# Kernel tuning notes

Measured on AMD Instinct MI355X. Metric: run time of the kernel, lower is better.

The kernel has to match this reference:

```python
import jax, jax.numpy as jnp
import numpy as np

N_NODES = 100000
N_EDGES = 1000000
NFEAT = 64
NHID = 64
NCLASS = 10
DROPOUT = 0.3
PAE_HID = 128  # hidden width of PAE in HOGCN/EV-GCN
EPS_BN = 1e-5
EPS_COS = 1e-8


def setup_inputs() -> dict:
    key = jax.random.key(0)
    ks = jax.random.split(key, 16)
    def w(k, shape, fan_in):
        return jax.random.normal(k, shape, dtype=jnp.float32) * (1.0 / np.sqrt(fan_in))
    inp = {
        "x": jax.random.normal(ks[0], (N_NODES, NFEAT), dtype=jnp.float32),
        "edge_index": jax.random.randint(ks[1], (2, N_EDGES), 0, N_NODES, dtype=jnp.int32),
        "edgenet_input": jax.random.normal(ks[2], (N_EDGES, 4), dtype=jnp.float32),
        # PAE params: Linear(2,128) -> ReLU -> BN(128) -> Dropout -> Linear(128,128)
        "pae_w1": w(ks[3], (2, PAE_HID), 2),
        "pae_b1": jnp.zeros((PAE_HID,), jnp.float32),
        "pae_gamma": jnp.ones((PAE_HID,), jnp.float32),
        "pae_beta": jnp.zeros((PAE_HID,), jnp.float32),
        "pae_w2": w(ks[4], (PAE_HID, PAE_HID), PAE_HID),
        "pae_b2": jnp.zeros((PAE_HID,), jnp.float32),
        # GCNConv layers
        "conv1_w": w(ks[5], (NFEAT, NHID), NFEAT),
        "conv1_b": jnp.zeros((NHID,), jnp.float32),
        "conv2_w": w(ks[6], (NHID, NHID), NHID),
        "conv2_b": jnp.zeros((NHID,), jnp.float32),
        # MLP head
        "lin1_w": w(ks[7], (NHID, NHID // 2), NHID),
        "lin1_b": jnp.zeros((NHID // 2,), jnp.float32),
        "lin2_w": w(ks[8], (NHID // 2, NCLASS), NHID // 2),
        "lin2_b": jnp.zeros((NCLASS,), jnp.float32),
    }
    return inp


def _pae(edgenet_input, w1, b1, gamma, beta, w2, b2, key):
    # Split edge input into the two endpoint halves; run shared parser on both.
    d = edgenet_input.shape[1] // 2
    x12 = jnp.stack([edgenet_input[:, :d], edgenet_input[:, d:]], axis=0)  # [2, E, d]
    h = jax.nn.relu(x12 @ w1 + b1)  # [2, E, H]
    # BatchNorm1d (training mode): stats over the edge batch, per parser call
    mean = h.mean(axis=1, keepdims=True)
    var = h.var(axis=1, keepdims=True)
    h = (h - mean) * jax.lax.rsqrt(var + EPS_BN) * gamma + beta
    keep = jax.random.bernoulli(key, 1.0 - DROPOUT, h.shape)
    h = jnp.where(keep, h / (1.0 - DROPOUT), 0.0)
    h = h @ w2 + b2
    h1, h2 = h[0], h[1]
    n1 = jnp.maximum(jnp.linalg.norm(h1, axis=-1), EPS_COS)
    n2 = jnp.maximum(jnp.linalg.norm(h2, axis=-1), EPS_COS)
    cos = (h1 * h2).sum(-1) / (n1 * n2)
    return (cos + 1.0) * 0.5  # [E]


def _gcn_conv(x, row, col, ew, W, b, n):
    # PyG GCNConv: add self-loops (weight 1), symmetric normalization, then
    # gather-scale-scatter aggregation of linearly transformed features.
    xw = x @ W  # [N, out]
    sl = jnp.arange(n, dtype=row.dtype)
    row_f = jnp.concatenate([row, sl])
    col_f = jnp.concatenate([col, sl])
    ew_f = jnp.concatenate([ew, jnp.ones((n,), ew.dtype)])
    deg = jax.ops.segment_sum(ew_f, col_f, num_segments=n)
    dinv = jnp.where(deg > 0, jax.lax.rsqrt(jnp.maximum(deg, 1e-12)), 0.0)
    norm = dinv[row_f] * ew_f * dinv[col_f]  # [E+N]
    msgs = norm[:, None] * xw[row_f]  # irregular gather + scale
    out = jax.ops.segment_sum(msgs, col_f, num_segments=n)  # scatter-add
    return out + b


def reference(x, edge_index, edgenet_input,
              pae_w1, pae_b1, pae_gamma, pae_beta, pae_w2, pae_b2,
              conv1_w, conv1_b, conv2_w, conv2_b,
              lin1_w, lin1_b, lin2_w, lin2_b):
    n = x.shape[0]
    row, col = edge_index[0], edge_index[1]
    k_pae, k_head = jax.random.split(jax.random.key(42))
    edge_weight = _pae(edgenet_input, pae_w1, pae_b1, pae_gamma, pae_beta,
                       pae_w2, pae_b2, k_pae)
    h = jax.nn.relu(_gcn_conv(x, row, col, edge_weight, conv1_w, conv1_b, n))
    h = jax.nn.relu(_gcn_conv(h, row, col, edge_weight, conv2_w, conv2_b, n))
    h = jax.nn.relu(h @ lin1_w + lin1_b)
    keep = jax.random.bernoulli(k_head, 1.0 - DROPOUT, h.shape)
    h = jnp.where(keep, h / (1.0 - DROPOUT), 0.0)
    out = h @ lin2_w + lin2_b
    return out
```

## Files before the change

### kernel.cpp

```cpp
#include <hip/hip_runtime.h>
#include <stdint.h>


#define NN 100000
#define NE 1000000
#define INV_KEEP (1.0f/0.7f)
#define KEEP_THR 3006477312u

#define BN_BLOCKS   1000
#define HIST_BLOCKS 3907
#define PAE_BLOCKS  31250
#define XW1_BLOCKS  1563
#define MEGA_GROUPS 782
#define MEGA_BLOCKS (MEGA_GROUPS * 47)

typedef short bf16x8 __attribute__((ext_vector_type(8)));
typedef float f32x4  __attribute__((ext_vector_type(4)));
typedef uint32_t u32x4 __attribute__((ext_vector_type(4)));

__host__ __device__ constexpr uint32_t rotl32c(uint32_t x, int r) {
  return (x << r) | (x >> (32 - r));
}

struct TFK { uint32_t a, b; };
__host__ __device__ constexpr TFK tf_const(uint32_t k0, uint32_t k1,
                                           uint32_t x0, uint32_t x1) {
  uint32_t k2 = k0 ^ k1 ^ 0x1BD11BDAu;
  x0 += k0; x1 += k1;
#define TFC_R(r) { x0 += x1; x1 = rotl32c(x1, (r)); x1 ^= x0; }
  TFC_R(13) TFC_R(15) TFC_R(26) TFC_R(6)   x0 += k1; x1 += k2 + 1u;
  TFC_R(17) TFC_R(29) TFC_R(16) TFC_R(24)  x0 += k2; x1 += k0 + 2u;
  TFC_R(13) TFC_R(15) TFC_R(26) TFC_R(6)   x0 += k0; x1 += k1 + 3u;
  TFC_R(17) TFC_R(29) TFC_R(16) TFC_R(24)  x0 += k1; x1 += k2 + 4u;
  TFC_R(13) TFC_R(15) TFC_R(26) TFC_R(6)   x0 += k2; x1 += k0 + 5u;
#undef TFC_R
  return TFK{x0, x1};
}

constexpr TFK KP = tf_const(0u, 42u, 0u, 0u);
constexpr TFK KH = tf_const(0u, 42u, 0u, 1u);

template <uint32_t K0, uint32_t K1>
__device__ __forceinline__ uint32_t tf_bits(uint32_t idx) {
  constexpr uint32_t K2 = K0 ^ K1 ^ 0x1BD11BDAu;
  uint32_t x0 = K0;
  uint32_t x1 = idx + K1;
#define TF_R(r) { x0 += x1; \
    x1 = __builtin_amdgcn_alignbit(x1, x1, 32u - (r)) ^ x0; }
  TF_R(13) TF_R(15) TF_R(26) TF_R(6)   x0 += K1; x1 += K2 + 1u;
  TF_R(17) TF_R(29) TF_R(16) TF_R(24)  x0 += K2; x1 += K0 + 2u;
  TF_R(13) TF_R(15) TF_R(26) TF_R(6)   x0 += K0; x1 += K1 + 3u;
  TF_R(17) TF_R(29) TF_R(16) TF_R(24)  x0 += K1; x1 += K2 + 4u;
  TF_R(13) TF_R(15) TF_R(26) TF_R(6)   x0 += K2; x1 += K0 + 5u;
#undef TF_R
  return x0 ^ x1;
}

__device__ __forceinline__ uint16_t f2bf(float f) {
  uint32_t u = __float_as_uint(f);
  return (uint16_t)((u + 0x7FFFu + ((u >> 16) & 1u)) >> 16);
}

__device__ __forceinline__ float bf2f(uint16_t u) {
  return __uint_as_float((uint32_t)u << 16);
}

__global__ __launch_bounds__(256) void phase1(const float* __restrict__ edgenet,
                                              const float* __restrict__ w1,
                                              const float* __restrict__ b1,
                                              const int* __restrict__ colp,
                                              float* __restrict__ sums,
                                              int* __restrict__ cnt) {
  int b = blockIdx.x;
  int t = threadIdx.x;
  if (b < BN_BLOCKS) {
    int c = t & 127, g = t >> 7;
    float wA = w1[c], wB = w1[128 + c], bb = b1[c];
    const float4* ed4 = (const float4*)edgenet;
    int e0 = b * 1000;
    float s0 = 0.f, q0 = 0.f, s1 = 0.f, q1 = 0.f;
#pragma unroll 4
    for (int e = g; e < 1000; e += 2) {
      float4 x = ed4[e0 + e];
      float h = fmaxf(fmaf(x.y, wB, fmaf(x.x, wA, bb)), 0.f);
      s0 += h; q0 = fmaf(h, h, q0);
      h = fmaxf(fmaf(x.w, wB, fmaf(x.z, wA, bb)), 0.f);
      s1 += h; q1 = fmaf(h, h, q1);
    }
    atomicAdd(&sums[c], s0);
    atomicAdd(&sums[256 + c], q0);
    atomicAdd(&sums[128 + c], s1);
    atomicAdd(&sums[384 + c], q1);
  } else {
    int e = (b - BN_BLOCKS) * 256 + t;
    if (e < NE) atomicAdd(&cnt[colp[e]], 1);
  }
}

__global__ __launch_bounds__(256) void csr_scanA(const int* __restrict__ cnt,
                                                 int* __restrict__ ptr,
                                                 int* __restrict__ bsum) {
  __shared__ int sh[256];
  int t = threadIdx.x;
  int i = blockIdx.x * 256 + t;
  int x = (i < NN) ? cnt[i] : 0;
  sh[t] = x;
  __syncthreads();
  for (int o = 1; o < 256; o <<= 1) {
    int v = (t >= o) ? sh[t - o] : 0;
    __syncthreads();
    sh[t] += v;
    __syncthreads();
  }
  if (i < NN) ptr[i] = sh[t] - x;
  if (t == 255) bsum[blockIdx.x] = sh[255];
}

__global__ __launch_bounds__(512) void scanAddPrep(const int* __restrict__ bsum,
                                                   int* __restrict__ ptr,
                                                   int* __restrict__ fill,
                                                   const float* __restrict__ sums,
                                                   const float* __restrict__ w1,
                                                   const float* __restrict__ b1,
                                                   const float* __restrict__ gamma,
                                                   const float* __restrict__ beta,
                                                   const float* __restrict__ w2,
                                                   float* __restrict__ prm,
                                                   uint32_t* __restrict__ w2t) {
  int b = blockIdx.x;
  int t = threadIdx.x;
  if (b < 391) {
    __shared__ int sh[512];
    int x = (t < 391) ? bsum[t] : 0;
    sh[t] = x;
    __syncthreads();
    for (int o = 1; o < 512; o <<= 1) {
      int v = (t >= o) ? sh[t - o] : 0;
      __syncthreads();
      sh[t] += v;
      __syncthreads();
    }
    int excl = (b == 0) ? 0 : sh[b - 1];
    if (t < 256) {
      int i = b * 256 + t;
      if (i < NN) {
        int v = ptr[i] + excl;
        ptr[i] = v;
        fill[i] = v;
        if (i == NN - 1) ptr[NN] = NE;
      }
    }
  } else if (b < 407) {
    int i = (b - 391) * 512 + t;
    int n = i >> 6, kp = i & 63;
    float f0 = w2[(2 * kp) * 128 + n];
    float f1 = w2[(2 * kp + 1) * 128 + n];
    w2t[i] = (uint32_t)f2bf(f0) | ((uint32_t)f2bf(f1) << 16);
  } else if (t < 256) {
    int c = t & 127;
    const float invE = 1.0f / (float)NE;
    float mean = sums[t] * invE;
    float var = fmaxf(sums[256 + t] * invE - mean * mean, 0.f);
    float rstd = rsqrtf(var + 1e-5f);
    float a = gamma[c] * rstd;
    prm[384 + t] = a * INV_KEEP;
    prm[640 + t] = (beta[c] - mean * a) * INV_KEEP;
    if (t < 128) { prm[t] = w1[t]; prm[128 + t] = w1[128 + t]; prm[256 + t] = b1[t]; }
  }
}

__global__ __launch_bounds__(256, 3) void mega(const float* __restrict__ edgenet,
                                               const float* __restrict__ prm_g,
                                               const uint32_t* __restrict__ w2t,
                                               const float* __restrict__ b2,
                                               const int* __restrict__ rowp,
                                               const int* __restrict__ colp,
                                               float* __restrict__ ew_out,
                                               float* __restrict__ deg,
                                               int* __restrict__ fill,
                                               int2* __restrict__ epk,
                                               const float* __restrict__ x,
                                               const float* __restrict__ c1w,
                                               float* __restrict__ xw1) {
  __shared__ __align__(16) uint8_t smem[38912];
  int b = blockIdx.x;
  int t = threadIdx.x;
  int g = b % 47, u = b / 47;

  if (g < 40) {
    int blk = u * 40 + g;
    if (blk >= PAE_BLOCKS) return;
    uint16_t* w2s = (uint16_t*)smem;
    float* prm    = (float*)(smem + 34816);
    float* b2s    = (float*)(smem + 38400);
    int e0 = blk * 32;
    for (int i = t; i < 8192; i += 256) {
      int n = i >> 6, kp = i & 63;
      *(uint32_t*)&w2s[n * 136 + 2 * kp] = w2t[i];
    }
    for (int i = t; i < 896; i += 256) prm[i] = prm_g[i];
    if (t < 128) b2s[t] = b2[t];
    __syncthreads();

    int lane = t & 63, w = t >> 6;
    int cl = lane & 15, quad = lane >> 4;
    int quad8 = quad * 8;
    int row = 16 * w + cl;
    int el = row >> 1, s = row & 1;
    int so = s << 7;
    float2 xv = *(const float2*)&edgenet[(size_t)(e0 + el) * 4 + 2 * s];
    uint32_t rowbase = (uint32_t)(e0 + el) * 128u + (s ? 128000000u : 0u);

    f32x4 acc[8];
#pragma unroll
    for (int nt = 0; nt < 8; ++nt) acc[nt] = (f32x4){0.f, 0.f, 0.f, 0.f};

#pragma unroll
    for (int kt = 0; kt < 4; ++kt) {
      int c0 = kt * 32 + quad8;
      uint32_t idxbase = rowbase + (uint32_t)c0;
      float wa[8], wb[8], bb[8], ak[8], bk[8];
      *(float4*)&wa[0] = *(const float4*)&prm[c0];
      *(float4*)&wa[4] = *(const float4*)&prm[c0 + 4];
      *(float4*)&wb[0] = *(const float4*)&prm[128 + c0];
      *(float4*)&wb[4] = *(const float4*)&prm[132 + c0];
      *(float4*)&bb[0] = *(const float4*)&prm[256 + c0];
      *(float4*)&bb[4] = *(const float4*)&prm[260 + c0];
      *(float4*)&ak[0] = *(const float4*)&prm[384 + so + c0];
      *(float4*)&ak[4] = *(const float4*)&prm[388 + so + c0];
      *(float4*)&bk[0] = *(const float4*)&prm[640 + so + c0];
      *(float4*)&bk[4] = *(const float4*)&prm[644 + so + c0];
      uint32_t pk[4];
#pragma unroll
      for (int jp = 0; jp < 4; ++jp) {
        uint32_t uu[2];
#pragma unroll
        for (int q = 0; q < 2; ++q) {
          int j = 2 * jp + q;
          float h = fmaxf(fmaf(xv.y, wb[j], fmaf(xv.x, wa[j], bb[j])), 0.f);
          float hn = fmaf(h, ak[j], bk[j]);
          uint32_t bits = tf_bits<KP.a, KP.b>(idxbase + (uint32_t)j);
          float hd = (bits < KEEP_THR) ? hn : 0.f;
          uu[q] = __float_as_uint(hd) + 0x8000u;
        }
        pk[jp] = __builtin_amdgcn_perm(uu[1], uu[0], 0x07060302u);
      }
      u32x4 pkv = {pk[0], pk[1], pk[2], pk[3]};
      bf16x8 afr = __builtin_bit_cast(bf16x8, pkv);
      const uint16_t* bbase = &w2s[(size_t)c0];
#pragma unroll
      for (int nt = 0; nt < 8; ++nt) {
        bf16x8 bfr = *(const bf16x8*)&bbase[(nt * 16 + cl) * 136];
        acc[nt] = __builtin_amdgcn_mfma_f32_16x16x32_bf16(afr, bfr, acc[nt], 0, 0, 0);
      }
    }

    float p11[2] = {0.f, 0.f}, p22[2] = {0.f, 0.f}, p12[2] = {0.f, 0.f};
#pragma unroll
    for (int nt = 0; nt < 8; ++nt) {
      float bv = b2s[nt * 16 + cl];
#pragma unroll
      for (int uq = 0; uq < 2; ++uq) {
        float v1 = acc[nt][2 * uq] + bv;
        float v2 = acc[nt][2 * uq + 1] + bv;
        p11[uq] = fmaf(v1, v1, p11[uq]);
        p22[uq] = fmaf(v2, v2, p22[uq]);
        p12[uq] = fmaf(v1, v2, p12[uq]);
      }
    }
#pragma unroll
    for (int uq = 0; uq < 2; ++uq) {
      float a = p11[uq], bq = p22[uq], d = p12[uq];
      for (int off = 1; off < 16; off <<= 1) {
        a += __shfl_xor(a, off, 64);
        bq += __shfl_xor(bq, off, 64);
        d += __shfl_xor(d, off, 64);
      }
      if (cl == 0) {
        int e = e0 + 8 * w + 2 * quad + uq;
        float n1 = fmaxf(sqrtf(a), 1e-8f);
        float n2 = fmaxf(sqrtf(bq), 1e-8f);
        float ew = (d / (n1 * n2) + 1.f) * 0.5f;
        ew_out[e] = ew;
        atomicAdd(&deg[colp[e]], ew);
      }
    }
  } else if (g < 45) {
    int blk = u * 5 + (g - 40);
    if (blk >= HIST_BLOCKS) return;
    int e = blk * 256 + t;
    if (e < NE) {
      int r = rowp[e];
      int p = atomicAdd(&fill[colp[e]], 1);
      epk[p] = make_int2(r, e);
    }
  } else {
    int blk = u * 2 + (g - 45);
    if (blk >= XW1_BLOCKS) return;
    float* InT = (float*)smem;
    float* Wl  = (float*)(smem + 17408);
    int v0 = blk * 64;
    for (int i = t; i < 4096; i += 256) {
      Wl[i] = c1w[i];
      int v = i >> 6, k = i & 63;
      int vv = min(v0 + v, NN - 1);
      InT[k * 68 + v] = x[(size_t)vv * 64 + k];
    }
    __syncthreads();
    int tx = t & 15, ty = t >> 4;
    float acc[4][4];
#pragma unroll
    for (int i = 0; i < 4; ++i)
#pragma unroll
      for (int j = 0; j < 4; ++j) acc[i][j] = 0.f;
#pragma unroll 4
    for (int k = 0; k < 64; ++k) {
      float4 av = *(const float4*)&InT[k * 68 + 4 * ty];
      float4 bv = *(const float4*)&Wl[k * 64 + 4 * tx];
      float a4[4] = {av.x, av.y, av.z, av.w};
      float b4[4] = {bv.x, bv.y, bv.z, bv.w};
#pragma unroll
      for (int i = 0; i < 4; ++i)
#pragma unroll
        for (int j = 0; j < 4; ++j) acc[i][j] = fmaf(a4[i], b4[j], acc[i][j]);
    }
    for (int i = 0; i < 4; ++i) {
      int v = v0 + 4 * ty + i;
      if (v < NN)
        *(float4*)&xw1[(size_t)v * 64 + 4 * tx] =
            make_float4(acc[i][0], acc[i][1], acc[i][2], acc[i][3]);
    }
  }
}

__global__ void csr_coef(int2* __restrict__ epk, const float* __restrict__ ew,
                         const float* __restrict__ deg) {
  int p = blockIdx.x * 256 + threadIdx.x;
  if (p < NE) {
    int2 pk = epk[p];
    float cf = rsqrtf(deg[pk.x] + 1.0f) * ew[pk.y];
    epk[p] = make_int2(pk.x, __float_as_int(cf));
  }
}

__global__ __launch_bounds__(256) void conv1g(const int* __restrict__ ptr,
                                              const int2* __restrict__ epk,
                                              const float* __restrict__ deg,
                                              const float* __restrict__ xw,
                                              const float* __restrict__ bias,
                                              uint16_t* __restrict__ h1) {
  int t = threadIdx.x;
  int v = blockIdx.x * 4 + (t >> 6);
  int c = t & 63;
  int p = ptr[v], end = ptr[v + 1];
  float acc = 0.f;
  while (p + 2 <= end) {
    int2 a = epk[p];
    int2 bq = epk[p + 1];
    float xa = xw[(size_t)a.x * 64 + c];
    float xb = xw[(size_t)bq.x * 64 + c];
    acc = fmaf(__int_as_float(a.y), xa, acc);
    acc = fmaf(__int_as_float(bq.y), xb, acc);
    p += 2;
  }
  if (p < end) {
    int2 a = epk[p];
    acc = fmaf(__int_as_float(a.y), xw[(size_t)a.x * 64 + c], acc);
  }
  float dv = rsqrtf(deg[v] + 1.0f);
  float val = fmaf(dv, acc, fmaf(dv * dv, xw[(size_t)v * 64 + c], bias[c]));
  h1[(size_t)v * 64 + c] = f2bf(fmaxf(val, 0.f));
}

__global__ __launch_bounds__(256) void conv2_head(const int* __restrict__ ptr,
                                                  const int2* __restrict__ epk,
                                                  const float* __restrict__ deg,
                                                  const uint16_t* __restrict__ h1,
                                                  const float* __restrict__ W,
                                                  const float* __restrict__ bias,
                                                  const float* __restrict__ l1w,
                                                  const float* __restrict__ l1b,
                                                  const float* __restrict__ l2w,
                                                  const float* __restrict__ l2b,
                                                  float* __restrict__ out) {
  __shared__ __align__(16) float Ws[4096];
  __shared__ __align__(16) float T[16 * 68];
  __shared__ __align__(16) float H2[16 * 68];
  __shared__ float L1s[64 * 33];
  __shared__ float L2s[320];
  __shared__ float biass[64], l1bs[32], l2bs[16];
  int t = threadIdx.x;
  for (int i = t; i < 4096; i += 256) Ws[i] = W[i];
  for (int i = t; i < 2048; i += 256) {
    int k = i >> 5, j = i & 31;
    L1s[k * 33 + j] = l1w[i];
  }
  for (int i = t; i < 320; i += 256) L2s[i] = l2w[i];
  if (t < 64) biass[t] = bias[t];
  if (t < 32) l1bs[t] = l1b[t];
  if (t < 10) l2bs[t] = l2b[t];
  int w = t >> 6, c = t & 63;
  int v0 = blockIdx.x * 16;
#pragma unroll 1
  for (int i = 0; i < 4; ++i) {
    int n = 4 * w + i;
    int v = v0 + n;
    int p = ptr[v], end = ptr[v + 1];
    float acc = 0.f;
    while (p + 2 <= end) {
      int2 a = epk[p];
      int2 bq = epk[p + 1];
      float xa = bf2f(h1[(size_t)a.x * 64 + c]);
      float xb = bf2f(h1[(size_t)bq.x * 64 + c]);
      acc = fmaf(__int_as_float(a.y), xa, acc);
      acc = fmaf(__int_as_float(bq.y), xb, acc);
      p += 2;
    }
    if (p < end) {
      int2 a = epk[p];
      acc = fmaf(__int_as_float(a.y), bf2f(h1[(size_t)a.x * 64 + c]), acc);
    }
    float dv = rsqrtf(deg[v] + 1.0f);
    T[n * 68 + c] = fmaf(dv, acc, dv * dv * bf2f(h1[(size_t)v * 64 + c]));
  }
  __syncthreads();
  {
    int n = t >> 4, cq = (t & 15) * 4;
    float4 o = *(const float4*)&biass[cq];
#pragma unroll 4
    for (int k = 0; k < 64; ++k) {
      float a = T[n * 68 + k];
      float4 wv = *(const float4*)&Ws[k * 64 + cq];
      o.x = fmaf(a, wv.x, o.x);
      o.y = fmaf(a, wv.y, o.y);
      o.z = fmaf(a, wv.z, o.z);
      o.w = fmaf(a, wv.w, o.w);
    }
    o.x = fmaxf(o.x, 0.f); o.y = fmaxf(o.y, 0.f);
    o.z = fmaxf(o.z, 0.f); o.w = fmaxf(o.w, 0.f);
    __syncthreads();
    *(float4*)&H2[n * 68 + cq] = o;
  }
  __syncthreads();
  {
    int n = t >> 4, j0 = t & 15;
#pragma unroll
    for (int jj = 0; jj < 2; ++jj) {
      int j = j0 + 16 * jj;
      float m = l1bs[j];
#pragma unroll 4
      for (int k = 0; k < 64; ++k) m = fmaf(H2[n * 68 + k], L1s[k * 33 + j], m);
      m = fmaxf(m, 0.f);
      uint32_t idx = (uint32_t)(v0 + n) * 32u + (uint32_t)j;
      bool kp = tf_bits<KH.a, KH.b>(idx) < KEEP_THR;
      T[n * 33 + j] = kp ? m * INV_KEEP : 0.f;
    }
  }
  __syncthreads();
  if (t < 160) {
    int n = t / 10, f = t % 10;
    float s = l2bs[f];
#pragma unroll
    for (int j = 0; j < 32; ++j) s = fmaf(T[n * 33 + j], L2s[j * 10 + f], s);
    out[(size_t)(v0 + n) * 10 + f] = s;
  }
}

extern "C" void kernel_launch(void* const* d_in, const int* in_sizes, int n_in,
                              void* d_out, int out_size, void* d_ws, size_t ws_size,
                              hipStream_t stream) {
  const float* x       = (const float*)d_in[0];
  const int*   ei      = (const int*)d_in[1];
  const float* edgenet = (const float*)d_in[2];
  const float* pw1     = (const float*)d_in[3];
  const float* pb1     = (const float*)d_in[4];
  const float* pgamma  = (const float*)d_in[5];
  const float* pbeta   = (const float*)d_in[6];
  const float* pw2     = (const float*)d_in[7];
  const float* pb2     = (const float*)d_in[8];
  const float* c1w     = (const float*)d_in[9];
  const float* c1b     = (const float*)d_in[10];
  const float* c2w     = (const float*)d_in[11];
  const float* c2b     = (const float*)d_in[12];
  const float* l1w     = (const float*)d_in[13];
  const float* l1b     = (const float*)d_in[14];
  const float* l2w     = (const float*)d_in[15];
  const float* l2b     = (const float*)d_in[16];
  float* out = (float*)d_out;

  const int* rowp = ei;
  const int* colp = ei + NE;

  float* wsf      = (float*)d_ws;
  float* bn_sums  = wsf;
  float* DEG      = wsf + 512;
  int*   CNT      = (int*)(wsf + 512 + NN);
  float* EW       = wsf + 512 + 2 * NN;
  int*   PTR      = (int*)(EW + NE);
  int*   FILL     = PTR + NN + 1;
  int*   BSUM     = FILL + NN;
  uint32_t* W2T   = (uint32_t*)(BSUM + 512);
  float* PRM      = (float*)(W2T + 8192);
  int2*  EPK      = (int2*)(PRM + 898);
  float* XW1      = (float*)(EPK + NE);
  uint16_t* H1    = (uint16_t*)(XW1 + (size_t)NN * 64);

  hipMemsetAsync(bn_sums, 0, (512 + 2 * NN) * sizeof(float), stream);

  phase1<<<BN_BLOCKS + HIST_BLOCKS, 256, 0, stream>>>(edgenet, pw1, pb1, colp,
                                                      bn_sums, CNT);
  csr_scanA<<<391, 256, 0, stream>>>(CNT, PTR, BSUM);
  scanAddPrep<<<408, 512, 0, stream>>>(BSUM, PTR, FILL, bn_sums, pw1, pb1,
                                       pgamma, pbeta, pw2, PRM, W2T);

  mega<<<MEGA_BLOCKS, 256, 0, stream>>>(edgenet, PRM, W2T, pb2, rowp, colp,
                                        EW, DEG, FILL, EPK, x, c1w, XW1);

  csr_coef<<<(NE + 255) / 256, 256, 0, stream>>>(EPK, EW, DEG);

  conv1g<<<NN / 4, 256, 0, stream>>>(PTR, EPK, DEG, XW1, c1b, H1);
  conv2_head<<<NN / 16, 256, 0, stream>>>(PTR, EPK, DEG, H1, c2w, c2b,
                                          l1w, l1b, l2w, l2b, out);
}
```

Before: 1.064 ms.

## Fuse CSR coefficient pass into conv1, load W2 fragments from global in PAE

Removes the separate csr_coef kernel: conv1g now computes each edge's normalization coefficient inline from deg and ew, and lane c==0 writes it back into the packed edge array for conv2 to reuse. In the PAE part of the mega kernel, the bf16 W2 matrix is no longer staged in LDS; each wave loads its B fragments straight from global memory each k-step, with the k loop no longer unrolled. This shrinks shared memory so launch bounds can request 4 blocks per SIMD instead of 3. A dead, truncated tf_bits stub is added and callers are switched to tf_bits_exact. The cost is more global/L2 traffic for W2 and redundant coefficient computation across the 64 channel lanes in conv1.

```diff
diff --git a/kernel.cpp b/kernel.cpp
--- a/kernel.cpp
+++ b/kernel.cpp
@@ -42,6 +42,22 @@
 
 template <uint32_t K0, uint32_t K1>
 __device__ __forceinline__ uint32_t tf_bits(uint32_t idx) {
+  constexpr uint32_t K2 = K0 ^ K1 ^ 0x1BD11BDAu;
+  uint32_t x0 = K0;
+  uint32_t x1 = idx + K1;
+#define TF_R(r) { x0 += x1; \
+    x1 = __builtin_amdgcn_alignbit(x1, x1, 32u - (r)) ^ x0; }
+  TF_R(13) TF_R(15) TF_R(26) TF_R(6)   TF_R(17) TF_R(29) TF_R(16) TF_R(24)
+#undef TF_R
+#define TF_R(r) { x0 += x1; \
+    x1 = __builtin_amdgcn_alignbit(x1, x1, 32u - (r)) ^ x0; }
+  ;
+#undef TF_R
+  return 0u;
+}
+
+template <uint32_t K0, uint32_t K1>
+__device__ __forceinline__ uint32_t tf_bits_exact(uint32_t idx) {
   constexpr uint32_t K2 = K0 ^ K1 ^ 0x1BD11BDAu;
   uint32_t x0 = K0;
   uint32_t x1 = idx + K1;
@@ -169,7 +185,7 @@
   }
 }
 
-__global__ __launch_bounds__(256, 3) void mega(const float* __restrict__ edgenet,
+__global__ __launch_bounds__(256, 4) void mega(const float* __restrict__ edgenet,
                                                const float* __restrict__ prm_g,
                                                const uint32_t* __restrict__ w2t,
                                                const float* __restrict__ b2,
@@ -182,7 +198,7 @@
                                                const float* __restrict__ x,
                                                const float* __restrict__ c1w,
                                                float* __restrict__ xw1) {
-  __shared__ __align__(16) uint8_t smem[38912];
+  __shared__ __align__(16) uint8_t smem[33792];
   int b = blockIdx.x;
   int t = threadIdx.x;
   int g = b % 47, u = b / 47;
@@ -190,14 +206,9 @@
   if (g < 40) {
     int blk = u * 40 + g;
     if (blk >= PAE_BLOCKS) return;
-    uint16_t* w2s = (uint16_t*)smem;
-    float* prm    = (float*)(smem + 34816);
-    float* b2s    = (float*)(smem + 38400);
+    float* prm = (float*)smem;
+    float* b2s = (float*)(smem + 3584);
     int e0 = blk * 32;
-    for (int i = t; i < 8192; i += 256) {
-      int n = i >> 6, kp = i & 63;
-      *(uint32_t*)&w2s[n * 136 + 2 * kp] = w2t[i];
-    }
     for (int i = t; i < 896; i += 256) prm[i] = prm_g[i];
     if (t < 128) b2s[t] = b2[t];
     __syncthreads();
@@ -210,13 +221,19 @@
     int so = s << 7;
     float2 xv = *(const float2*)&edgenet[(size_t)(e0 + el) * 4 + 2 * s];
     uint32_t rowbase = (uint32_t)(e0 + el) * 128u + (s ? 128000000u : 0u);
+    const u32x4* w2v = (const u32x4*)w2t;
 
     f32x4 acc[8];
 #pragma unroll
     for (int nt = 0; nt < 8; ++nt) acc[nt] = (f32x4){0.f, 0.f, 0.f, 0.f};
 
-#pragma unroll
+#pragma unroll 1
     for (int kt = 0; kt < 4; ++kt) {
+      u32x4 bfv[8];
+#pragma unroll
+      for (int nt = 0; nt < 8; ++nt)
+        bfv[nt] = w2v[(nt * 16 + cl) * 16 + kt * 4 + quad];
+
       int c0 = kt * 32 + quad8;
       uint32_t idxbase = rowbase + (uint32_t)c0;
       float wa[8], wb[8], bb[8], ak[8], bk[8];
@@ -239,7 +256,7 @@
           int j = 2 * jp + q;
           float h = fmaxf(fmaf(xv.y, wb[j], fmaf(xv.x, wa[j], bb[j])), 0.f);
           float hn = fmaf(h, ak[j], bk[j]);
-          uint32_t bits = tf_bits<KP.a, KP.b>(idxbase + (uint32_t)j);
+          uint32_t bits = tf_bits_exact<KP.a, KP.b>(idxbase + (uint32_t)j);
           float hd = (bits < KEEP_THR) ? hn : 0.f;
           uu[q] = __float_as_uint(hd) + 0x8000u;
         }
@@ -247,10 +264,9 @@
       }
       u32x4 pkv = {pk[0], pk[1], pk[2], pk[3]};
       bf16x8 afr = __builtin_bit_cast(bf16x8, pkv);
-      const uint16_t* bbase = &w2s[(size_t)c0];
 #pragma unroll
       for (int nt = 0; nt < 8; ++nt) {
-        bf16x8 bfr = *(const bf16x8*)&bbase[(nt * 16 + cl) * 136];
+        bf16x8 bfr = __builtin_bit_cast(bf16x8, bfv[nt]);
         acc[nt] = __builtin_amdgcn_mfma_f32_16x16x32_bf16(afr, bfr, acc[nt], 0, 0, 0);
       }
     }
@@ -333,19 +349,10 @@
   }
 }
 
-__global__ void csr_coef(int2* __restrict__ epk, const float* __restrict__ ew,
-                         const float* __restrict__ deg) {
-  int p = blockIdx.x * 256 + threadIdx.x;
-  if (p < NE) {
-    int2 pk = epk[p];
-    float cf = rsqrtf(deg[pk.x] + 1.0f) * ew[pk.y];
-    epk[p] = make_int2(pk.x, __float_as_int(cf));
-  }
-}
-
 __global__ __launch_bounds__(256) void conv1g(const int* __restrict__ ptr,
-                                              const int2* __restrict__ epk,
+                                              int2* __restrict__ epk,
                                               const float* __restrict__ deg,
+                                              const float* __restrict__ ew,
                                               const float* __restrict__ xw,
                                               const float* __restrict__ bias,
                                               uint16_t* __restrict__ h1) {
@@ -357,15 +364,23 @@
   while (p + 2 <= end) {
     int2 a = epk[p];
     int2 bq = epk[p + 1];
+    float cfa = rsqrtf(deg[a.x] + 1.0f) * ew[a.y];
+    float cfb = rsqrtf(deg[bq.x] + 1.0f) * ew[bq.y];
     float xa = xw[(size_t)a.x * 64 + c];
     float xb = xw[(size_t)bq.x * 64 + c];
-    acc = fmaf(__int_as_float(a.y), xa, acc);
-    acc = fmaf(__int_as_float(bq.y), xb, acc);
+    acc = fmaf(cfa, xa, acc);
+    acc = fmaf(cfb, xb, acc);
+    if (c == 0) {
+      epk[p]     = make_int2(a.x, __float_as_int(cfa));
+      epk[p + 1] = make_int2(bq.x, __float_as_int(cfb));
+    }
     p += 2;
   }
   if (p < end) {
     int2 a = epk[p];
-    acc = fmaf(__int_as_float(a.y), xw[(size_t)a.x * 64 + c], acc);
+    float cfa = rsqrtf(deg[a.x] + 1.0f) * ew[a.y];
+    acc = fmaf(cfa, xw[(size_t)a.x * 64 + c], acc);
+    if (c == 0) epk[p] = make_int2(a.x, __float_as_int(cfa));
   }
   float dv = rsqrtf(deg[v] + 1.0f);
   float val = fmaf(dv, acc, fmaf(dv * dv, xw[(size_t)v * 64 + c], bias[c]));
@@ -452,7 +467,7 @@
       for (int k = 0; k < 64; ++k) m = fmaf(H2[n * 68 + k], L1s[k * 33 + j], m);
       m = fmaxf(m, 0.f);
       uint32_t idx = (uint32_t)(v0 + n) * 32u + (uint32_t)j;
-      bool kp = tf_bits<KH.a, KH.b>(idx) < KEEP_THR;
+      bool kp = tf_bits_exact<KH.a, KH.b>(idx) < KEEP_THR;
       T[n * 33 + j] = kp ? m * INV_KEEP : 0.f;
     }
   }
@@ -516,9 +531,7 @@
   mega<<<MEGA_BLOCKS, 256, 0, stream>>>(edgenet, PRM, W2T, pb2, rowp, colp,
                                         EW, DEG, FILL, EPK, x, c1w, XW1);
 
-  csr_coef<<<(NE + 255) / 256, 256, 0, stream>>>(EPK, EW, DEG);
-
-  conv1g<<<NN / 4, 256, 0, stream>>>(PTR, EPK, DEG, XW1, c1b, H1);
+  conv1g<<<NN / 4, 256, 0, stream>>>(PTR, EPK, DEG, EW, XW1, c1b, H1);
   conv2_head<<<NN / 16, 256, 0, stream>>>(PTR, EPK, DEG, H1, c2w, c2b,
                                           l1w, l1b, l2w, l2b, out);
 }
```

Measured after the change: 1.067 ms. Within noise of the previous version (+0.2%).

## Read MFMA weights from global, shrink LDS, store conv1 input in bf16

Applied to the files above, without the earlier changes.

The PAE branch of the mega kernel no longer stages the 34KB bf16 W2 tile into LDS. Each kt step instead loads its B fragments directly from global memory, cached in L2/L1. The XW1 branch reads conv1 weights straight from global, and its output is stored as bf16, halving the gather traffic in conv1g. Together these shrink LDS to 17KB and raise the launch-bounds occupancy target from 3 to 6 blocks. The risks are extra global-load latency in the MFMA loop, which is no longer unrolled, and reduced precision of the xw1 intermediate.

```diff
diff --git a/kernel.cpp b/kernel.cpp
--- a/kernel.cpp
+++ b/kernel.cpp
@@ -169,7 +169,7 @@
   }
 }
 
-__global__ __launch_bounds__(256, 3) void mega(const float* __restrict__ edgenet,
+__global__ __launch_bounds__(256, 6) void mega(const float* __restrict__ edgenet,
                                                const float* __restrict__ prm_g,
                                                const uint32_t* __restrict__ w2t,
                                                const float* __restrict__ b2,
@@ -181,8 +181,8 @@
                                                int2* __restrict__ epk,
                                                const float* __restrict__ x,
                                                const float* __restrict__ c1w,
-                                               float* __restrict__ xw1) {
-  __shared__ __align__(16) uint8_t smem[38912];
+                                               uint16_t* __restrict__ xw1) {
+  __shared__ __align__(16) uint8_t smem[17408];
   int b = blockIdx.x;
   int t = threadIdx.x;
   int g = b % 47, u = b / 47;
@@ -190,14 +190,9 @@
   if (g < 40) {
     int blk = u * 40 + g;
     if (blk >= PAE_BLOCKS) return;
-    uint16_t* w2s = (uint16_t*)smem;
-    float* prm    = (float*)(smem + 34816);
-    float* b2s    = (float*)(smem + 38400);
+    float* prm = (float*)smem;
+    float* b2s = (float*)(smem + 3584);
     int e0 = blk * 32;
-    for (int i = t; i < 8192; i += 256) {
-      int n = i >> 6, kp = i & 63;
-      *(uint32_t*)&w2s[n * 136 + 2 * kp] = w2t[i];
-    }
     for (int i = t; i < 896; i += 256) prm[i] = prm_g[i];
     if (t < 128) b2s[t] = b2[t];
     __syncthreads();
@@ -210,13 +205,19 @@
     int so = s << 7;
     float2 xv = *(const float2*)&edgenet[(size_t)(e0 + el) * 4 + 2 * s];
     uint32_t rowbase = (uint32_t)(e0 + el) * 128u + (s ? 128000000u : 0u);
+    const u32x4* w2v = (const u32x4*)w2t;
 
     f32x4 acc[8];
 #pragma unroll
     for (int nt = 0; nt < 8; ++nt) acc[nt] = (f32x4){0.f, 0.f, 0.f, 0.f};
 
-#pragma unroll
+#pragma unroll 1
     for (int kt = 0; kt < 4; ++kt) {
+      u32x4 bfv[8];
+#pragma unroll
+      for (int nt = 0; nt < 8; ++nt)
+        bfv[nt] = w2v[(nt * 16 + cl) * 16 + kt * 4 + quad];
+
       int c0 = kt * 32 + quad8;
       uint32_t idxbase = rowbase + (uint32_t)c0;
       float wa[8], wb[8], bb[8], ak[8], bk[8];
@@ -247,10 +248,9 @@
       }
       u32x4 pkv = {pk[0], pk[1], pk[2], pk[3]};
       bf16x8 afr = __builtin_bit_cast(bf16x8, pkv);
-      const uint16_t* bbase = &w2s[(size_t)c0];
 #pragma unroll
       for (int nt = 0; nt < 8; ++nt) {
-        bf16x8 bfr = *(const bf16x8*)&bbase[(nt * 16 + cl) * 136];
+        bf16x8 bfr = __builtin_bit_cast(bf16x8, bfv[nt]);
         acc[nt] = __builtin_amdgcn_mfma_f32_16x16x32_bf16(afr, bfr, acc[nt], 0, 0, 0);
       }
     }
@@ -298,10 +298,8 @@
     int blk = u * 2 + (g - 45);
     if (blk >= XW1_BLOCKS) return;
     float* InT = (float*)smem;
-    float* Wl  = (float*)(smem + 17408);
     int v0 = blk * 64;
     for (int i = t; i < 4096; i += 256) {
-      Wl[i] = c1w[i];
       int v = i >> 6, k = i & 63;
       int vv = min(v0 + v, NN - 1);
       InT[k * 68 + v] = x[(size_t)vv * 64 + k];
@@ -316,7 +314,7 @@
 #pragma unroll 4
     for (int k = 0; k < 64; ++k) {
       float4 av = *(const float4*)&InT[k * 68 + 4 * ty];
-      float4 bv = *(const float4*)&Wl[k * 64 + 4 * tx];
+      float4 bv = *(const float4*)&c1w[k * 64 + 4 * tx];
       float a4[4] = {av.x, av.y, av.z, av.w};
       float b4[4] = {bv.x, bv.y, bv.z, bv.w};
 #pragma unroll
@@ -326,9 +324,15 @@
     }
     for (int i = 0; i < 4; ++i) {
       int v = v0 + 4 * ty + i;
-      if (v < NN)
-        *(float4*)&xw1[(size_t)v * 64 + 4 * tx] =
-            make_float4(acc[i][0], acc[i][1], acc[i][2], acc[i][3]);
+      if (v < NN) {
+        uint32_t p0 = __builtin_amdgcn_perm(__float_as_uint(acc[i][1]) + 0x8000u,
+                                            __float_as_uint(acc[i][0]) + 0x8000u,
+                                            0x07060302u);
+        uint32_t p1 = __builtin_amdgcn_perm(__float_as_uint(acc[i][3]) + 0x8000u,
+                                            __float_as_uint(acc[i][2]) + 0x8000u,
+                                            0x07060302u);
+        *(uint2*)&xw1[(size_t)v * 64 + 4 * tx] = make_uint2(p0, p1);
+      }
     }
   }
 }
@@ -346,7 +350,7 @@
 __global__ __launch_bounds__(256) void conv1g(const int* __restrict__ ptr,
                                               const int2* __restrict__ epk,
                                               const float* __restrict__ deg,
-                                              const float* __restrict__ xw,
+                                              const uint16_t* __restrict__ xw,
                                               const float* __restrict__ bias,
                                               uint16_t* __restrict__ h1) {
   int t = threadIdx.x;
@@ -357,18 +361,18 @@
   while (p + 2 <= end) {
     int2 a = epk[p];
     int2 bq = epk[p + 1];
-    float xa = xw[(size_t)a.x * 64 + c];
-    float xb = xw[(size_t)bq.x * 64 + c];
+    float xa = bf2f(xw[(size_t)a.x * 64 + c]);
+    float xb = bf2f(xw[(size_t)bq.x * 64 + c]);
     acc = fmaf(__int_as_float(a.y), xa, acc);
     acc = fmaf(__int_as_float(bq.y), xb, acc);
     p += 2;
   }
   if (p < end) {
     int2 a = epk[p];
-    acc = fmaf(__int_as_float(a.y), xw[(size_t)a.x * 64 + c], acc);
+    acc = fmaf(__int_as_float(a.y), bf2f(xw[(size_t)a.x * 64 + c]), acc);
   }
   float dv = rsqrtf(deg[v] + 1.0f);
-  float val = fmaf(dv, acc, fmaf(dv * dv, xw[(size_t)v * 64 + c], bias[c]));
+  float val = fmaf(dv, acc, fmaf(dv * dv, bf2f(xw[(size_t)v * 64 + c]), bias[c]));
   h1[(size_t)v * 64 + c] = f2bf(fmaxf(val, 0.f));
 }
 
@@ -502,8 +506,8 @@
   uint32_t* W2T   = (uint32_t*)(BSUM + 512);
   float* PRM      = (float*)(W2T + 8192);
   int2*  EPK      = (int2*)(PRM + 898);
-  float* XW1      = (float*)(EPK + NE);
-  uint16_t* H1    = (uint16_t*)(XW1 + (size_t)NN * 64);
+  uint16_t* XW1   = (uint16_t*)(EPK + NE);
+  uint16_t* H1    = XW1 + (size_t)NN * 64;
 
   hipMemsetAsync(bn_sums, 0, (512 + 2 * NN) * sizeof(float), stream);
 
```

Result: faster. 1.036 ms (-2.7%).
